# Kernel tuning notes

Hardware: AMD Instinct MI355X
Metric: run time of the kernel (lower is better)

Reference implementation:

```python
import jax, jax.numpy as jnp
import numpy as np

ND, NPR, DD, DP, LAT, AT, B = 2048, 2048, 128, 128, 128, 32, 16384


def setup_inputs():
    key = jax.random.key(0)
    ks = jax.random.split(key, 20)
    s = 0.05
    d = {}
    d["e_p_adj"] = (jax.random.uniform(ks[0], (ND, NPR)) < 0.05).astype(jnp.float32)
    d["e_e_adj"] = (jax.random.uniform(ks[1], (ND, ND)) < 0.05).astype(jnp.float32)
    d["p_p_adj"] = (jax.random.uniform(ks[2], (NPR, NPR)) < 0.05).astype(jnp.float32)
    d["input_disease"] = jax.random.randint(ks[3], (B,), 0, ND)
    d["input_drug"] = jax.random.randint(ks[4], (B,), 0, NPR)
    d["labels"] = jax.random.randint(ks[5], (B,), 0, 2)
    # learned parameters
    d["disease_emb"] = jax.random.normal(ks[6], (ND, DD)) * s
    d["drug_emb"] = jax.random.normal(ks[7], (NPR, DP)) * s
    d["Wdg"] = jax.random.normal(ks[8], (DP, LAT)) * s   # disease_gcn_w
    d["bdg_lin"] = jnp.zeros((LAT,))                      # Linear bias
    d["bdg"] = jnp.zeros((LAT,))                          # extra disease_gcn_b
    d["Wpg"] = jax.random.normal(ks[9], (DD, LAT)) * s   # drug_gcn_w
    d["bpg_lin"] = jnp.zeros((LAT,))
    d["bpg"] = jnp.zeros((LAT,))
    d["Wa1_d"] = jax.random.normal(ks[10], (DP + DD, AT)) * s  # concat [key(drug), query(disease)]
    d["ba1_d"] = jnp.zeros((AT,))
    d["Wa2_d"] = jax.random.normal(ks[11], (AT, 1)) * s
    d["ba2_d"] = jnp.zeros((1,))
    d["Wa1_p"] = jax.random.normal(ks[12], (DD + DP, AT)) * s  # concat [key(disease), query(drug)]
    d["ba1_p"] = jnp.zeros((AT,))
    d["Wa2_p"] = jax.random.normal(ks[13], (AT, 1)) * s
    d["ba2_p"] = jnp.zeros((1,))
    d["Wd2"] = jax.random.normal(ks[14], (DD, LAT)) * s  # disease_w2
    d["bd2"] = jnp.zeros((LAT,))
    d["Wp3"] = jax.random.normal(ks[15], (DP, LAT)) * s  # drug_w3
    d["bp3"] = jnp.zeros((LAT,))
    d["mlp_W1"] = jax.random.normal(ks[16], (LAT, DD)) * s
    d["mlp_b1"] = jnp.zeros((DD,))
    d["mlp_W2"] = jax.random.normal(ks[17], (DD, DD)) * s
    d["mlp_b2"] = jnp.zeros((DD,))
    d["Wpred"] = jax.random.normal(ks[18], (DD, 1)) * s
    d["bpred"] = jnp.zeros((1,))
    return d


def _attention_gcn(adj, other, selfe, W1, b1, W2, b2):
    # torch: concat([key=other, query=self]) -> Linear(W1) ; split W1 instead of
    # materializing the [Ns, No, Dk+Dq] concat tensor (same math, less HBM traffic)
    do = other.shape[1]
    ko = other @ W1[:do]              # [No, A]
    qs = selfe @ W1[do:]              # [Ns, A]
    h = jax.nn.relu(qs[:, None, :] + ko[None, :, :] + b1)   # [Ns, No, A]
    alpha = jax.nn.relu(jnp.squeeze(h @ W2, -1) + b2[0])    # [Ns, No]
    alpha = alpha * adj
    return jax.nn.softmax(alpha, axis=1) @ other            # [Ns, Do]


def _forward(e_p_adj, e_e_adj, p_p_adj, input_disease, input_drug, labels,
             disease_emb, drug_emb, Wdg, bdg_lin, bdg, Wpg, bpg_lin, bpg,
             Wa1_d, ba1_d, Wa2_d, ba2_d, Wa1_p, ba1_p, Wa2_p, ba2_p,
             Wd2, bd2, Wp3, bp3, mlp_W1, mlp_b1, mlp_W2, mlp_b2, Wpred, bpred):
    h_e_gcn = _attention_gcn(e_p_adj, drug_emb, disease_emb, Wa1_d, ba1_d, Wa2_d, ba2_d)
    h_e_gcn = h_e_gcn @ Wdg + bdg_lin + bdg
    h_p_gcn = _attention_gcn(e_p_adj.T, disease_emb, drug_emb, Wa1_p, ba1_p, Wa2_p, ba2_p)
    h_p_gcn = h_p_gcn @ Wpg + bpg_lin + bpg
    # disease knn branch
    deg_d = jnp.sum(e_e_adj, axis=1, keepdims=True) + 1e-8
    h_e_e = ((e_e_adj @ disease_emb) / deg_d) @ Wd2 + bd2
    h_e = jax.nn.selu(h_e_gcn + h_e_e)
    # drug knn branch
    deg_p = jnp.sum(p_p_adj, axis=1, keepdims=True) + 1e-8
    h_p_p = ((p_p_adj @ drug_emb) / deg_p) @ Wp3 + bp3
    h_p = jax.nn.selu(h_p_gcn + h_p_p)
    # pair prediction MLP
    x = h_e[input_disease] * h_p[input_drug]                # [B, LAT]
    x = jax.nn.selu(x @ mlp_W1 + mlp_b1)
    x = jax.nn.selu(x @ mlp_W2 + mlp_b2)
    z = jnp.squeeze(x @ Wpred, -1) + bpred[0]               # [B]
    y = labels.astype(jnp.float32)
    # BCEWithLogitsLoss (stable), mean reduction
    loss = jnp.mean(jnp.maximum(z, 0.0) - z * y + jnp.log1p(jnp.exp(-jnp.abs(z))))
    return (loss, jax.nn.sigmoid(z))


def reference(e_p_adj, e_e_adj, p_p_adj, input_disease, input_drug, labels,
              disease_emb, drug_emb, Wdg, bdg_lin, bdg, Wpg, bpg_lin, bpg,
              Wa1_d, ba1_d, Wa2_d, ba2_d, Wa1_p, ba1_p, Wa2_p, ba2_p,
              Wd2, bd2, Wp3, bp3, mlp_W1, mlp_b1, mlp_W2, mlp_b2, Wpred, bpred):
    return _forward(e_p_adj, e_e_adj, p_p_adj, input_disease, input_drug, labels,
                    disease_emb, drug_emb, Wdg, bdg_lin, bdg, Wpg, bpg_lin, bpg,
                    Wa1_d, ba1_d, Wa2_d, ba2_d, Wa1_p, ba1_p, Wa2_p, ba2_p,
                    Wd2, bd2, Wp3, bp3, mlp_W1, mlp_b1, mlp_W2, mlp_b2, Wpred, bpred)
```

## Files before the change

kernel.cpp:

```cpp
#include <hip/hip_runtime.h>

#define ND   2048
#define BB   16384

typedef unsigned short u16;
typedef unsigned int u32;
typedef __attribute__((ext_vector_type(8))) short short8;
typedef __attribute__((ext_vector_type(4))) float f32x4;

__device__ inline float bf2f(u16 u) {
    union { u32 i; float f; } v; v.i = ((u32)u) << 16; return v.f;
}
__device__ inline u16 f2bf(float f) {
    union { float f; u32 i; } v; v.f = f;
    u32 i = v.i + 0x7fffu + ((v.i >> 16) & 1u);
    return (u16)(i >> 16);
}
__device__ inline float seluf(float x) {
    const float sc = 1.0507009873554805f, al = 1.6732632423543772f;
    return x > 0.f ? sc * x : sc * al * expm1f(x);
}

__global__ void detectk(const void* __restrict__ demb, u32* __restrict__ flag,
                        u32* __restrict__ cntT) {
    const u16* p = (const u16*)demb;
    int tid = threadIdx.x;
    #pragma unroll
    for (int i = 0; i < 8; i++) cntT[i * 256 + tid] = 0u;
    int sane = 0;
    #pragma unroll
    for (int i = 0; i < 2; i++) {
        u16 u = p[4 * tid + 2 * i];
        int e = (u >> 7) & 0xFF;
        if (u == 0 || (e >= 0x66 && e <= 0x8C)) sane++;
    }
    __shared__ int red[256];
    red[tid] = sane; __syncthreads();
    for (int o = 128; o > 0; o >>= 1) {
        if (tid < o) red[tid] += red[tid + o];
        __syncthreads();
    }
    if (tid == 0) flag[0] = (red[0] < 300) ? 1u : 0u;
}

#define NSEG 26
struct CvtArgs { const void* src[NSEG]; int off[NSEG]; int n[NSEG]; };
struct CS {
    const void* adj[3];
    u16* ridx[3]; u32* rcnt[3];
};

__global__ __launch_bounds__(256) void cvtcsr(CvtArgs a, u16* __restrict__ base,
                                              CS c, const u32* __restrict__ flag) {
    int bx = blockIdx.x;
    int t = threadIdx.x;
    bool f32 = flag[0] != 0;
    if (bx < 6144) {
        int m = bx >> 11, r = bx & 2047;
        int lane = t & 63;
        __shared__ u32 lcnt;
        if (t == 0) lcnt = 0;
        __syncthreads();
        float v[8];
        int c0 = t * 8;
        if (f32) {
            const float4* p = (const float4*)((const float*)c.adj[m] + (size_t)r * 2048 + c0);
            float4 x = p[0], y = p[1];
            v[0] = x.x; v[1] = x.y; v[2] = x.z; v[3] = x.w;
            v[4] = y.x; v[5] = y.y; v[6] = y.z; v[7] = y.w;
        } else {
            const uint4* p = (const uint4*)((const u16*)c.adj[m] + (size_t)r * 2048 + c0);
            uint4 x = p[0];
            u32 u[4] = {x.x, x.y, x.z, x.w};
            #pragma unroll
            for (int i = 0; i < 4; i++) {
                v[2 * i + 0] = (u[i] & 0xffffu) ? 1.f : 0.f;
                v[2 * i + 1] = (u[i] >> 16)     ? 1.f : 0.f;
            }
        }
        int cnt = 0;
        #pragma unroll
        for (int i = 0; i < 8; i++) cnt += (v[i] != 0.f) ? 1 : 0;
        int pfx = cnt;
        #pragma unroll
        for (int o = 1; o < 64; o <<= 1) {
            int s = __shfl_up(pfx, o, 64);
            if (lane >= o) pfx += s;
        }
        int wtot = __shfl(pfx, 63, 64);
        u32 wb = 0;
        if (lane == 0) wb = atomicAdd(&lcnt, (u32)wtot);
        wb = __shfl((int)wb, 0, 64);
        int o = (int)wb + pfx - cnt;
        u16* ridx = c.ridx[m] + (size_t)r * 2048;
        #pragma unroll
        for (int i = 0; i < 8; i++) {
            if (v[i] != 0.f) ridx[o++] = (u16)(c0 + i);
        }
        __syncthreads();
        if (t == 0) c.rcnt[m][r] = lcnt;
    } else {
        int idx = bx - 6144;
        int seg = idx >> 6, xb = idx & 63;
        int n = a.n[seg];
        const void* s = a.src[seg];
        u16* d = base + a.off[seg];
        for (int i = xb * 256 + t; i < n; i += 16384)
            d[i] = f32 ? f2bf(((const float*)s)[i]) : ((const u16*)s)[i];
    }
}

struct PR {
    const u16* demb; const u16* pemb;
    const u16* Wa1d; const u16* ba1d;
    const u16* Wa1p; const u16* ba1p;
    float* ko_d; float* qs_d; float* ko_p; float* qs_p;
    const u16* idx0; const u32* cnt0; u16* cidx; u32* ccnt;
    const u16* ts[6]; u16* W1T; u16* W2T; u16* WcTe; u16* WcTp;
    float* cspart;
    const u16* ba[3]; const u16* bb[3]; u16* b_e; u16* b_p;
    float* csd; float* csp;
};

__global__ __launch_bounds__(256) void prep2(PR p) {
    int bx = blockIdx.x;
    int tid = threadIdx.x;
    __shared__ float sx[2][128];
    __shared__ float sred[2][128];
    __shared__ u16 stile[32][33];
    __shared__ float st0[256], st1[256];

    if (bx < 4096) {
        int sub = tid >> 7, t = tid & 127;
        int unit = bx * 2 + sub;
        int row = unit & 2047, m = unit >> 11;
        const u16* src; const u16* W; const u16* bias; float* out;
        switch (m) {
            case 0:  src = p.pemb; W = p.Wa1d;            bias = nullptr; out = p.ko_d; break;
            case 1:  src = p.demb; W = p.Wa1d + 128 * 32; bias = p.ba1d;  out = p.qs_d; break;
            case 2:  src = p.demb; W = p.Wa1p;            bias = nullptr; out = p.ko_p; break;
            default: src = p.pemb; W = p.Wa1p + 128 * 32; bias = p.ba1p;  out = p.qs_p; break;
        }
        sx[sub][t] = bf2f(src[(size_t)row * 128 + t]);
        __syncthreads();
        int a = t & 31, part = t >> 5;
        float s = 0.f;
        #pragma unroll
        for (int k = 0; k < 32; k++)
            s += sx[sub][part * 32 + k] * bf2f(W[(part * 32 + k) * 32 + a]);
        sred[sub][t] = s;
        __syncthreads();
        if (part == 0) {
            float tt = sred[sub][a] + sred[sub][a + 32] + sred[sub][a + 64] + sred[sub][a + 96];
            if (bias) tt += bf2f(bias[a]);
            out[(size_t)row * 32 + a] = tt;
        }
    } else if (bx < 6144) {
        int r = bx - 4096;
        int n = (int)p.cnt0[r];
        const u16* row = p.idx0 + (size_t)r * 2048;
        for (int i = tid; i < n; i += 256) {
            int cc = (int)row[i];
            u32 q = atomicAdd(&p.ccnt[cc], 1u);
            p.cidx[(size_t)cc * 2048 + q] = (u16)r;
        }
    } else if (bx < 6240) {
        int id = bx - 6144;
        int z = id >> 4, rem = id & 15;
        int c0 = (rem & 3) * 32, r0 = (rem >> 2) * 32;
        const u16* in = p.ts[z];
        u16* out; int ldo, ooff;
        switch (z) {
            case 0:  out = p.W1T;  ldo = 128; ooff = 0;   break;
            case 1:  out = p.W2T;  ldo = 128; ooff = 0;   break;
            case 2:  out = p.WcTe; ldo = 256; ooff = 0;   break;
            case 3:  out = p.WcTe; ldo = 256; ooff = 128; break;
            case 4:  out = p.WcTp; ldo = 256; ooff = 0;   break;
            default: out = p.WcTp; ldo = 256; ooff = 128; break;
        }
        int tx = tid & 31, ty = tid >> 5;
        int x = c0 + tx;
        for (int i = ty; i < 32; i += 8)
            stile[i][tx] = in[(size_t)(r0 + i) * 128 + x];
        __syncthreads();
        int rr = r0 + tx;
        for (int i = ty; i < 32; i += 8)
            out[(size_t)(c0 + i) * ldo + ooff + rr] = stile[tx][i];
    } else if (bx < 6304) {
        int id = bx - 6240;
        int m = id >> 5, xb = id & 31;
        const u16* e = m ? p.pemb : p.demb;
        int c2 = tid & 63, rg = tid >> 6;
        int r0 = xb * 64;
        float s0 = 0.f, s1 = 0.f;
        for (int i = 0; i < 16; i++) {
            u32 v = *(const u32*)(e + (size_t)(r0 + i * 4 + rg) * 128 + c2 * 2);
            s0 += bf2f((u16)(v & 0xffffu));
            s1 += bf2f((u16)(v >> 16));
        }
        st0[tid] = s0; st1[tid] = s1;
        __syncthreads();
        if (tid < 64) {
            float a0 = st0[tid] + st0[tid + 64] + st0[tid + 128] + st0[tid + 192];
            float a1 = st1[tid] + st1[tid + 64] + st1[tid + 128] + st1[tid + 192];
            p.cspart[(size_t)m * 4096 + xb * 128 + tid * 2 + 0] = a0;
            p.cspart[(size_t)m * 4096 + xb * 128 + tid * 2 + 1] = a1;
        }
    } else {
    }
}

__global__ void biasfin(PR p) {
    int t = threadIdx.x;
    p.b_e[t] = f2bf(bf2f(p.ba[0][t]) + bf2f(p.ba[1][t]) + bf2f(p.ba[2][t]));
    p.b_p[t] = f2bf(bf2f(p.bb[0][t]) + bf2f(p.bb[1][t]) + bf2f(p.bb[2][t]));
    float sd = 0.f, sp = 0.f;
    for (int b = 0; b < 32; b++) {
        sd += p.cspart[b * 128 + t];
        sp += p.cspart[4096 + b * 128 + t];
    }
    p.csd[t] = sd;
    p.csp[t] = sp;
}

struct SP {
    const u16* idx[4]; const u32* cnt[4];
    const float* ko[4]; const float* qs[4];
    const u16* w2[4]; const u16* b2[4];
    const u16* emb[4]; const float* csum[4];
    u16* out[4]; int ooff[4]; int attn[4];
};

__global__ __launch_bounds__(256) void spagg(SP a) {
    int task = blockIdx.y;
    int tid = threadIdx.x;
    int wv = tid >> 6, lane = tid & 63;
    int grp = lane >> 4, dim = lane & 15;
    int r = blockIdx.x * 4 + wv;
    const u16* idx = a.idx[task] + (size_t)r * 2048;
    int nnz = (int)a.cnt[task][r];
    int isat = a.attn[task];
    const u16* emb = a.emb[task];
    const float* ko = a.ko[task];

    float qsr[32], w2h[32];
    float b2v = 0.f;
    if (isat) {
        const float4* qp = (const float4*)(a.qs[task] + (size_t)r * 32);
        #pragma unroll
        for (int i = 0; i < 8; i++) {
            float4 v = qp[i];
            qsr[4 * i + 0] = v.x; qsr[4 * i + 1] = v.y;
            qsr[4 * i + 2] = v.z; qsr[4 * i + 3] = v.w;
        }
        #pragma unroll
        for (int i = 0; i < 32; i++) w2h[i] = bf2f(a.w2[task][i]);
        b2v = bf2f(a.b2[task][0]);
    }

    float acc[8];
    #pragma unroll
    for (int t = 0; t < 8; t++) acc[t] = 0.f;
    float wsuml = 0.f;

    for (int base = 0; base < nnz; base += 64) {
        int i = base + lane;
        float w = 0.f;
        int j = 0;
        if (i < nnz) {
            j = (int)idx[i];
            if (isat) {
                const float4* kp = (const float4*)(ko + (size_t)j * 32);
                float s = 0.f;
                #pragma unroll
                for (int q = 0; q < 8; q++) {
                    float4 kv = kp[q];
                    s += fmaxf(qsr[4 * q + 0] + kv.x, 0.f) * w2h[4 * q + 0];
                    s += fmaxf(qsr[4 * q + 1] + kv.y, 0.f) * w2h[4 * q + 1];
                    s += fmaxf(qsr[4 * q + 2] + kv.z, 0.f) * w2h[4 * q + 2];
                    s += fmaxf(qsr[4 * q + 3] + kv.w, 0.f) * w2h[4 * q + 3];
                }
                w = __expf(fmaxf(s + b2v, 0.f)) - 1.f;
                wsuml += w;
            }
        }
        int cend = min(64, nnz - base);
        #pragma unroll 4
        for (int k4 = 0; k4 < cend; k4 += 4) {
            int kk = k4 + grp;
            int jk = __shfl(j, kk, 64);
            float wk = isat ? __shfl(w, kk, 64)
                            : ((base + kk < nnz) ? 1.f : 0.f);
            const uint4* pp = (const uint4*)((const char*)emb + jk * 256 + dim * 16);
            uint4 vv = *pp;
            u32 u[4] = {vv.x, vv.y, vv.z, vv.w};
            #pragma unroll
            for (int cc = 0; cc < 4; cc++) {
                acc[2 * cc + 0] = fmaf(wk, bf2f((u16)(u[cc] & 0xffffu)), acc[2 * cc + 0]);
                acc[2 * cc + 1] = fmaf(wk, bf2f((u16)(u[cc] >> 16)), acc[2 * cc + 1]);
            }
        }
    }

    #pragma unroll
    for (int t = 0; t < 8; t++) {
        acc[t] += __shfl_xor(acc[t], 32, 64);
        acc[t] += __shfl_xor(acc[t], 16, 64);
    }
    if (isat) {
        #pragma unroll
        for (int o = 32; o > 0; o >>= 1) wsuml += __shfl_xor(wsuml, o, 64);
    }

    if (grp == 0) {
        float v[8];
        if (isat) {
            float sc = 1.f / (2048.f + wsuml);
            const float* cs = a.csum[task] + dim * 8;
            #pragma unroll
            for (int t = 0; t < 8; t++) v[t] = (cs[t] + acc[t]) * sc;
        } else {
            float sc = 1.f / ((float)nnz + 1e-8f);
            #pragma unroll
            for (int t = 0; t < 8; t++) v[t] = acc[t] * sc;
        }
        uint4 pk;
        pk.x = (u32)f2bf(v[0]) | ((u32)f2bf(v[1]) << 16);
        pk.y = (u32)f2bf(v[2]) | ((u32)f2bf(v[3]) << 16);
        pk.z = (u32)f2bf(v[4]) | ((u32)f2bf(v[5]) << 16);
        pk.w = (u32)f2bf(v[6]) | ((u32)f2bf(v[7]) << 16);
        *(uint4*)(a.out[task] + (size_t)r * 256 + a.ooff[task] + dim * 8) = pk;
    }
}

struct GD4 {
    const void* A[4]; const u16* BT[4]; u16* C[4];
    const u16* bias[4]; const float* rs[4];
    int lda[4], ldb[4], ldc[4], coff[4], kiters[4], act[4], araw[4], rsmode[4];
};

#define PADK 136

__global__ __launch_bounds__(256, 2) void gemmL(GD4 g, const u32* __restrict__ flag) {
    __shared__ __align__(16) u16 As[16][PADK];
    __shared__ __align__(16) u16 Bs[128][PADK];
    int z = blockIdx.y;
    const void* A = g.A[z];
    const u16* BT = g.BT[z];
    int lda = g.lda[z], ldb = g.ldb[z];
    int kiters = g.kiters[z];
    int tid = threadIdx.x;
    int lane = tid & 63, wv = tid >> 6;
    int mrow = lane & 15, quad = lane >> 4;
    int m0 = blockIdx.x * 16;
    int c0 = wv * 32;
    int sr = tid >> 4, sk = (tid & 15) * 8;
    f32x4 acc0 = {0.f, 0.f, 0.f, 0.f}, acc1 = {0.f, 0.f, 0.f, 0.f};

    short8 ra, rb[8];
    auto ldstage = [&](int kb) {
        ra = *(const short8*)((const u16*)A + (size_t)(m0 + sr) * lda + kb + sk);
        const u16* bbase = BT + (size_t)sr * ldb + kb + sk;
        #pragma unroll
        for (int i = 0; i < 8; i++)
            rb[i] = *(const short8*)(bbase + (size_t)i * 16 * ldb);
    };
    auto ststage = [&]() {
        *(short8*)(&As[sr][sk]) = ra;
        #pragma unroll
        for (int i = 0; i < 8; i++)
            *(short8*)(&Bs[i * 16 + sr][sk]) = rb[i];
    };
    auto compute = [&]() {
        #pragma unroll
        for (int ks = 0; ks < 4; ks++) {
            short8 af = *(const short8*)(&As[mrow][ks * 32 + quad * 8]);
            short8 b0 = *(const short8*)(&Bs[c0 + mrow][ks * 32 + quad * 8]);
            short8 b1 = *(const short8*)(&Bs[c0 + 16 + mrow][ks * 32 + quad * 8]);
            acc0 = __builtin_amdgcn_mfma_f32_16x16x32_bf16(af, b0, acc0, 0, 0, 0);
            acc1 = __builtin_amdgcn_mfma_f32_16x16x32_bf16(af, b1, acc1, 0, 0, 0);
        }
    };

    ldstage(0);
    #pragma unroll 1
    for (int it = 0; it < kiters - 1; ++it) {
        ststage();
        __syncthreads();
        ldstage((it + 1) * 128);
        compute();
        __syncthreads();
    }
    ststage();
    __syncthreads();
    compute();

    const float* rs = g.rs[z];
    int rsmode = g.rsmode[z];
    const u16* bi = g.bias[z];
    u16* C = g.C[z];
    int ldc = g.ldc[z], coff = g.coff[z], act = g.act[z];
    int n0 = c0 + mrow, n1 = n0 + 16;
    float bv0 = bi ? bf2f(bi[n0]) : 0.f;
    float bv1 = bi ? bf2f(bi[n1]) : 0.f;
    #pragma unroll
    for (int r = 0; r < 4; r++) {
        int row = m0 + quad * 4 + r;
        float v0 = acc0[r], v1 = acc1[r];
        if (rsmode == 1) { float sc = rs[row]; v0 *= sc; v1 *= sc; }
        else if (rsmode == 2) {
            float t = 0.f;
            #pragma unroll
            for (int p = 0; p < 8; p++) t += rs[row + p * 2048];
            float sc = 1.f / t;
            v0 *= sc; v1 *= sc;
        }
        v0 += bv0; v1 += bv1;
        if (act) { v0 = seluf(v0); v1 = seluf(v1); }
        C[(size_t)row * ldc + coff + n0] = f2bf(v0);
        C[(size_t)row * ldc + coff + n1] = f2bf(v1);
    }
}

#define PADX 136
__global__ __launch_bounds__(256, 2) void mlpfused(
    const u16* __restrict__ he, const u16* __restrict__ hp,
    const int* __restrict__ di, const int* __restrict__ dr,
    const u16* __restrict__ W1T, const u16* __restrict__ b1,
    const u16* __restrict__ W2T, const u16* __restrict__ b2,
    const u16* __restrict__ wpred, const u16* __restrict__ bpred,
    const int* __restrict__ labels,
    float* __restrict__ out, float* __restrict__ part) {
    __shared__ __align__(16) u16 Xs[64][PADX];
    __shared__ __align__(16) u16 Ws[128][PADX];
    __shared__ float wred[4];
    int tid = threadIdx.x;
    int lane = tid & 63, wv = tid >> 6;
    int mrow = lane & 15, quad = lane >> 4;
    int p0 = blockIdx.x * 64;

    {
        int row = tid >> 2, sub = tid & 3;
        int b = p0 + row;
        int ia = di[b], ic = dr[b];
        const uint4* pe = (const uint4*)(he + (size_t)ia * 128 + sub * 32);
        const uint4* pp = (const uint4*)(hp + (size_t)ic * 128 + sub * 32);
        #pragma unroll
        for (int q = 0; q < 4; q++) {
            uint4 ue = pe[q], up = pp[q];
            u32 eu[4] = {ue.x, ue.y, ue.z, ue.w};
            u32 pu[4] = {up.x, up.y, up.z, up.w};
            #pragma unroll
            for (int c = 0; c < 4; c++) {
                float lo = bf2f((u16)(eu[c] & 0xffffu)) * bf2f((u16)(pu[c] & 0xffffu));
                float hi = bf2f((u16)(eu[c] >> 16)) * bf2f((u16)(pu[c] >> 16));
                *(u32*)(&Xs[row][sub * 32 + q * 8 + c * 2]) =
                    (u32)f2bf(lo) | ((u32)f2bf(hi) << 16);
            }
        }
    }
    {
        int n = tid >> 1, half = tid & 1;
        const short8* src = (const short8*)(W1T + (size_t)n * 128 + half * 64);
        short8* dst = (short8*)(&Ws[n][half * 64]);
        #pragma unroll
        for (int i = 0; i < 8; i++) dst[i] = src[i];
    }
    __syncthreads();

    f32x4 acc[8];
    #pragma unroll
    for (int nt = 0; nt < 8; nt++) acc[nt] = {0.f, 0.f, 0.f, 0.f};
    #pragma unroll
    for (int ks = 0; ks < 4; ks++) {
        short8 af = *(const short8*)(&Xs[wv * 16 + mrow][ks * 32 + quad * 8]);
        #pragma unroll
        for (int nt = 0; nt < 8; nt++) {
            short8 bfv = *(const short8*)(&Ws[nt * 16 + mrow][ks * 32 + quad * 8]);
            acc[nt] = __builtin_amdgcn_mfma_f32_16x16x32_bf16(af, bfv, acc[nt], 0, 0, 0);
        }
    }
    __syncthreads();
    #pragma unroll
    for (int nt = 0; nt < 8; nt++) {
        int col = nt * 16 + mrow;
        float bv = bf2f(b1[col]);
        #pragma unroll
        for (int r = 0; r < 4; r++) {
            int row = wv * 16 + quad * 4 + r;
            Xs[row][col] = f2bf(seluf(acc[nt][r] + bv));
        }
    }
    {
        int n = tid >> 1, half = tid & 1;
        const short8* src = (const short8*)(W2T + (size_t)n * 128 + half * 64);
        short8* dst = (short8*)(&Ws[n][half * 64]);
        #pragma unroll
        for (int i = 0; i < 8; i++) dst[i] = src[i];
    }
    __syncthreads();

    #pragma unroll
    for (int nt = 0; nt < 8; nt++) acc[nt] = {0.f, 0.f, 0.f, 0.f};
    #pragma unroll
    for (int ks = 0; ks < 4; ks++) {
        short8 af = *(const short8*)(&Xs[wv * 16 + mrow][ks * 32 + quad * 8]);
        #pragma unroll
        for (int nt = 0; nt < 8; nt++) {
            short8 bfv = *(const short8*)(&Ws[nt * 16 + mrow][ks * 32 + quad * 8]);
            acc[nt] = __builtin_amdgcn_mfma_f32_16x16x32_bf16(af, bfv, acc[nt], 0, 0, 0);
        }
    }

    float zp[4] = {0.f, 0.f, 0.f, 0.f};
    #pragma unroll
    for (int nt = 0; nt < 8; nt++) {
        int col = nt * 16 + mrow;
        float bv = bf2f(b2[col]);
        float wp = bf2f(wpred[col]);
        #pragma unroll
        for (int r = 0; r < 4; r++) {
            float x2 = bf2f(f2bf(seluf(acc[nt][r] + bv)));
            zp[r] = fmaf(x2, wp, zp[r]);
        }
    }
    #pragma unroll
    for (int r = 0; r < 4; r++) {
        #pragma unroll
        for (int o = 1; o < 16; o <<= 1) zp[r] += __shfl_xor(zp[r], o, 64);
    }
    float bpv = bf2f(bpred[0]);
    float lsum = 0.f;
    #pragma unroll
    for (int r = 0; r < 4; r++) {
        int b = p0 + wv * 16 + quad * 4 + r;
        float z = zp[r] + bpv;
        float sig = 1.f / (1.f + __expf(-z));
        if (mrow == 0) out[1 + b] = sig;
        float y = (float)labels[b];
        lsum += fmaxf(z, 0.f) - z * y + log1pf(__expf(-fabsf(z)));
    }
    lsum += __shfl_xor(lsum, 16, 64);
    lsum += __shfl_xor(lsum, 32, 64);
    if (lane == 0) wred[wv] = lsum;
    __syncthreads();
    if (tid == 0) part[blockIdx.x] = wred[0] + wred[1] + wred[2] + wred[3];
}

__global__ void finloss(const float* __restrict__ part, float* __restrict__ out) {
    __shared__ float s[256];
    int t = threadIdx.x;
    s[t] = part[t];
    __syncthreads();
    for (int o = 128; o > 0; o >>= 1) {
        if (t < o) s[t] += s[t + o];
        __syncthreads();
    }
    if (t == 0) out[0] = s[0] * (1.f / 16384.f);
}

extern "C" void kernel_launch(void* const* d_in, const int* in_sizes, int n_in,
                              void* d_out, int out_size, void* d_ws, size_t ws_size,
                              hipStream_t stream) {
    const void* e_p_adj = d_in[0];
    const void* e_e_adj = d_in[1];
    const void* p_p_adj = d_in[2];
    const int* in_dis  = (const int*)d_in[3];
    const int* in_drug = (const int*)d_in[4];
    const int* labels  = (const int*)d_in[5];
    float* out = (float*)d_out;

    char* ws = (char*)d_ws;
    size_t off = 0;
    auto take = [&](size_t bytes) { char* p = ws + off; off = (off + bytes + 255) & ~(size_t)255; return p; };
    u16*   A_e   = (u16*)take((size_t)2048 * 256 * 2);
    u16*   A_p   = (u16*)take((size_t)2048 * 256 * 2);
    u16*   WcTe  = (u16*)take((size_t)128 * 256 * 2);
    u16*   WcTp  = (u16*)take((size_t)128 * 256 * 2);
    u16*   W1T   = (u16*)take((size_t)128 * 128 * 2);
    u16*   W2T   = (u16*)take((size_t)128 * 128 * 2);
    u16*   b_e   = (u16*)take(256);
    u16*   b_p   = (u16*)take(256);
    u16*   h_e   = (u16*)take((size_t)2048 * 128 * 2);
    u16*   h_p   = (u16*)take((size_t)2048 * 128 * 2);
    float* ko_d  = (float*)take((size_t)2048 * 32 * 4);
    float* qs_d  = (float*)take((size_t)2048 * 32 * 4);
    float* ko_p  = (float*)take((size_t)2048 * 32 * 4);
    float* qs_p  = (float*)take((size_t)2048 * 32 * 4);
    float* cspart = (float*)take((size_t)2 * 32 * 128 * 4);
    float* csd   = (float*)take(128 * 4);
    float* csp   = (float*)take(128 * 4);
    float* part  = (float*)take(256 * 4);
    u32*   flag  = (u32*)take(256);
    u16*   canon = (u16*)take((size_t)700000 * 2);
    u16*   idx0  = (u16*)take((size_t)2048 * 2048 * 2);
    u16*   idx1  = (u16*)take((size_t)2048 * 2048 * 2);
    u16*   idx2  = (u16*)take((size_t)2048 * 2048 * 2);
    u16*   idx3  = (u16*)take((size_t)2048 * 2048 * 2);
    u32*   cnt0  = (u32*)take(2048 * 4);
    u32*   cnt2  = (u32*)take(2048 * 4);
    u32*   cnt3  = (u32*)take(2048 * 4);
    u32*   cntT  = (u32*)take(2048 * 4);

    const int segidx[NSEG] = {6, 7, 14, 18, 8, 22, 11, 24, 26, 28,
                              15, 16, 17, 19, 20, 21,
                              9, 10, 12, 13, 23, 25, 27, 29, 30, 31};
    const int segn[NSEG]   = {262144, 262144, 8192, 8192, 16384, 16384, 16384, 16384, 16384, 16384,
                              32, 32, 1, 32, 32, 1,
                              128, 128, 128, 128, 128, 128, 128, 128, 128, 1};
    CvtArgs ca;
    u16* cp[NSEG];
    {
        int o = 0;
        for (int i = 0; i < NSEG; i++) {
            ca.src[i] = d_in[segidx[i]];
            ca.off[i] = o;
            ca.n[i] = segn[i];
            cp[i] = canon + o;
            o += (segn[i] + 15) & ~15;
        }
    }
    u16 *cdemb = cp[0], *cpemb = cp[1], *cWa1d = cp[2], *cWa1p = cp[3];
    u16 *cWdg = cp[4], *cWd2 = cp[5], *cWpg = cp[6], *cWp3 = cp[7];
    u16 *cW1 = cp[8], *cW2 = cp[9];
    u16 *cba1d = cp[10], *cWa2d = cp[11], *cba2d = cp[12];
    u16 *cba1p = cp[13], *cWa2p = cp[14], *cba2p = cp[15];
    u16 *cbdg_lin = cp[16], *cbdg = cp[17], *cbpg_lin = cp[18], *cbpg = cp[19];
    u16 *cbd2 = cp[20], *cbp3 = cp[21], *cmb1 = cp[22], *cmb2 = cp[23];
    u16 *cWpred = cp[24], *cbpred = cp[25];

    detectk<<<1, 256, 0, stream>>>(d_in[6], flag, cntT);

    {
        CS cs;
        cs.adj[0] = e_p_adj; cs.ridx[0] = idx0; cs.rcnt[0] = cnt0;
        cs.adj[1] = e_e_adj; cs.ridx[1] = idx2; cs.rcnt[1] = cnt2;
        cs.adj[2] = p_p_adj; cs.ridx[2] = idx3; cs.rcnt[2] = cnt3;
        cvtcsr<<<6144 + 64 * NSEG, 256, 0, stream>>>(ca, canon, cs, flag);
    }

    PR pr;
    pr.demb = cdemb; pr.pemb = cpemb;
    pr.Wa1d = cWa1d; pr.ba1d = cba1d; pr.Wa1p = cWa1p; pr.ba1p = cba1p;
    pr.ko_d = ko_d; pr.qs_d = qs_d; pr.ko_p = ko_p; pr.qs_p = qs_p;
    pr.idx0 = idx0; pr.cnt0 = cnt0; pr.cidx = idx1; pr.ccnt = cntT;
    pr.ts[0] = cW1; pr.ts[1] = cW2; pr.ts[2] = cWdg;
    pr.ts[3] = cWd2; pr.ts[4] = cWpg; pr.ts[5] = cWp3;
    pr.W1T = W1T; pr.W2T = W2T; pr.WcTe = WcTe; pr.WcTp = WcTp;
    pr.cspart = cspart;
    pr.ba[0] = cbdg_lin; pr.ba[1] = cbdg; pr.ba[2] = cbd2;
    pr.bb[0] = cbpg_lin; pr.bb[1] = cbpg; pr.bb[2] = cbp3;
    pr.b_e = b_e; pr.b_p = b_p; pr.csd = csd; pr.csp = csp;
    prep2<<<6304, 256, 0, stream>>>(pr);
    biasfin<<<1, 128, 0, stream>>>(pr);

    {
        SP sp;
        sp.idx[0] = idx0; sp.cnt[0] = cnt0; sp.ko[0] = ko_d; sp.qs[0] = qs_d;
        sp.w2[0] = cWa2d; sp.b2[0] = cba2d; sp.emb[0] = cpemb; sp.csum[0] = csp;
        sp.out[0] = A_e; sp.ooff[0] = 0; sp.attn[0] = 1;
        sp.idx[1] = idx2; sp.cnt[1] = cnt2; sp.ko[1] = ko_d; sp.qs[1] = qs_d;
        sp.w2[1] = cWa2d; sp.b2[1] = cba2d; sp.emb[1] = cdemb; sp.csum[1] = csd;
        sp.out[1] = A_e; sp.ooff[1] = 128; sp.attn[1] = 0;
        sp.idx[2] = idx1; sp.cnt[2] = cntT; sp.ko[2] = ko_p; sp.qs[2] = qs_p;
        sp.w2[2] = cWa2p; sp.b2[2] = cba2p; sp.emb[2] = cdemb; sp.csum[2] = csd;
        sp.out[2] = A_p; sp.ooff[2] = 0; sp.attn[2] = 1;
        sp.idx[3] = idx3; sp.cnt[3] = cnt3; sp.ko[3] = ko_p; sp.qs[3] = qs_p;
        sp.w2[3] = cWa2p; sp.b2[3] = cba2p; sp.emb[3] = cpemb; sp.csum[3] = csp;
        sp.out[3] = A_p; sp.ooff[3] = 128; sp.attn[3] = 0;
        spagg<<<dim3(512, 4), 256, 0, stream>>>(sp);
    }

    auto setd = [](GD4& g, int z, const void* A, int lda, const u16* BT, int ldb,
                   u16* C, int ldc, int coff, int ki, const u16* bi,
                   const float* rs, int act, int araw, int rm) {
        g.A[z] = A; g.lda[z] = lda; g.BT[z] = BT; g.ldb[z] = ldb;
        g.C[z] = C; g.ldc[z] = ldc; g.coff[z] = coff; g.kiters[z] = ki;
        g.bias[z] = bi; g.rs[z] = rs; g.act[z] = act; g.araw[z] = araw; g.rsmode[z] = rm;
    };

    {
        GD4 g;
        setd(g, 0, A_e, 256, WcTe, 256, h_e, 128, 0, 2, b_e, nullptr, 1, 0, 0);
        setd(g, 1, A_p, 256, WcTp, 256, h_p, 128, 0, 2, b_p, nullptr, 1, 0, 0);
        setd(g, 2, A_e, 256, WcTe, 256, h_e, 128, 0, 2, b_e, nullptr, 1, 0, 0);
        setd(g, 3, A_e, 256, WcTe, 256, h_e, 128, 0, 2, b_e, nullptr, 1, 0, 0);
        gemmL<<<dim3(128, 2), 256, 0, stream>>>(g, flag);
    }

    mlpfused<<<256, 256, 0, stream>>>(h_e, h_p, in_dis, in_drug,
                                      W1T, cmb1, W2T, cmb2,
                                      cWpred, cbpred, labels, out, part);
    finloss<<<1, 256, 0, stream>>>(part, out);
}
```

Before: 236.5 us.

## Fold averaging into prep, batch CSR rows, merge bias/loss finalize kernels

Each CSR-conversion block now handles four adjacency rows instead of one, so the grid shrinks. The non-attention mean aggregations (e_e, p_p) move out of spagg into extra prep2 blocks, leaving spagg with only the two attention tasks. The biasfin kernel is folded into prep2, which now computes column sums in a single pass. The finloss kernel is replaced by an atomic accumulate plus last-block-finishes pattern inside mlpfused. Together these cut kernel launches and idle tails, at the cost of atomic ordering subtleties and a less deterministic loss summation.

```diff
diff --git a/kernel.cpp b/kernel.cpp
--- a/kernel.cpp
+++ b/kernel.cpp
@@ -22,11 +22,13 @@
 }
 
 __global__ void detectk(const void* __restrict__ demb, u32* __restrict__ flag,
-                        u32* __restrict__ cntT) {
+                        u32* __restrict__ cntT, float* __restrict__ lossacc,
+                        u32* __restrict__ losscnt) {
     const u16* p = (const u16*)demb;
     int tid = threadIdx.x;
     #pragma unroll
     for (int i = 0; i < 8; i++) cntT[i * 256 + tid] = 0u;
+    if (tid == 0) { lossacc[0] = 0.f; losscnt[0] = 0u; }
     int sane = 0;
     #pragma unroll
     for (int i = 0; i < 2; i++) {
@@ -55,52 +57,64 @@
     int bx = blockIdx.x;
     int t = threadIdx.x;
     bool f32 = flag[0] != 0;
-    if (bx < 6144) {
-        int m = bx >> 11, r = bx & 2047;
+    if (bx < 1536) {
+        int m = bx >> 9;
+        int r0 = (bx & 511) * 4;
         int lane = t & 63;
-        __shared__ u32 lcnt;
-        if (t == 0) lcnt = 0;
-        __syncthreads();
-        float v[8];
+        __shared__ u32 lcnt[4];
+        if (t < 4) lcnt[t] = 0;
+        __syncthreads();
+        float v[4][8];
         int c0 = t * 8;
         if (f32) {
-            const float4* p = (const float4*)((const float*)c.adj[m] + (size_t)r * 2048 + c0);
-            float4 x = p[0], y = p[1];
-            v[0] = x.x; v[1] = x.y; v[2] = x.z; v[3] = x.w;
-            v[4] = y.x; v[5] = y.y; v[6] = y.z; v[7] = y.w;
+            #pragma unroll
+            for (int rr = 0; rr < 4; rr++) {
+                const float4* p = (const float4*)((const float*)c.adj[m] +
+                                                  (size_t)(r0 + rr) * 2048 + c0);
+                float4 x = p[0], y = p[1];
+                v[rr][0] = x.x; v[rr][1] = x.y; v[rr][2] = x.z; v[rr][3] = x.w;
+                v[rr][4] = y.x; v[rr][5] = y.y; v[rr][6] = y.z; v[rr][7] = y.w;
+            }
         } else {
-            const uint4* p = (const uint4*)((const u16*)c.adj[m] + (size_t)r * 2048 + c0);
-            uint4 x = p[0];
-            u32 u[4] = {x.x, x.y, x.z, x.w};
-            #pragma unroll
-            for (int i = 0; i < 4; i++) {
-                v[2 * i + 0] = (u[i] & 0xffffu) ? 1.f : 0.f;
-                v[2 * i + 1] = (u[i] >> 16)     ? 1.f : 0.f;
+            #pragma unroll
+            for (int rr = 0; rr < 4; rr++) {
+                const uint4* p = (const uint4*)((const u16*)c.adj[m] +
+                                                (size_t)(r0 + rr) * 2048 + c0);
+                uint4 x = p[0];
+                u32 u[4] = {x.x, x.y, x.z, x.w};
+                #pragma unroll
+                for (int i = 0; i < 4; i++) {
+                    v[rr][2 * i + 0] = (u[i] & 0xffffu) ? 1.f : 0.f;
+                    v[rr][2 * i + 1] = (u[i] >> 16)     ? 1.f : 0.f;
+                }
             }
         }
-        int cnt = 0;
-        #pragma unroll
-        for (int i = 0; i < 8; i++) cnt += (v[i] != 0.f) ? 1 : 0;
-        int pfx = cnt;
-        #pragma unroll
-        for (int o = 1; o < 64; o <<= 1) {
-            int s = __shfl_up(pfx, o, 64);
-            if (lane >= o) pfx += s;
-        }
-        int wtot = __shfl(pfx, 63, 64);
-        u32 wb = 0;
-        if (lane == 0) wb = atomicAdd(&lcnt, (u32)wtot);
-        wb = __shfl((int)wb, 0, 64);
-        int o = (int)wb + pfx - cnt;
-        u16* ridx = c.ridx[m] + (size_t)r * 2048;
-        #pragma unroll
-        for (int i = 0; i < 8; i++) {
-            if (v[i] != 0.f) ridx[o++] = (u16)(c0 + i);
-        }
-        __syncthreads();
-        if (t == 0) c.rcnt[m][r] = lcnt;
+        #pragma unroll
+        for (int rr = 0; rr < 4; rr++) {
+            int cnt = 0;
+            #pragma unroll
+            for (int i = 0; i < 8; i++) cnt += (v[rr][i] != 0.f) ? 1 : 0;
+            int pfx = cnt;
+            #pragma unroll
+            for (int o = 1; o < 64; o <<= 1) {
+                int s = __shfl_up(pfx, o, 64);
+                if (lane >= o) pfx += s;
+            }
+            int wtot = __shfl(pfx, 63, 64);
+            u32 wb = 0;
+            if (lane == 0) wb = atomicAdd(&lcnt[rr], (u32)wtot);
+            wb = __shfl((int)wb, 0, 64);
+            int o = (int)wb + pfx - cnt;
+            u16* ridx = c.ridx[m] + (size_t)(r0 + rr) * 2048;
+            #pragma unroll
+            for (int i = 0; i < 8; i++) {
+                if (v[rr][i] != 0.f) ridx[o++] = (u16)(c0 + i);
+            }
+        }
+        __syncthreads();
+        if (t < 4) c.rcnt[m][r0 + t] = lcnt[t];
     } else {
-        int idx = bx - 6144;
+        int idx = bx - 1536;
         int seg = idx >> 6, xb = idx & 63;
         int n = a.n[seg];
         const void* s = a.src[seg];
@@ -117,9 +131,9 @@
     float* ko_d; float* qs_d; float* ko_p; float* qs_p;
     const u16* idx0; const u32* cnt0; u16* cidx; u32* ccnt;
     const u16* ts[6]; u16* W1T; u16* W2T; u16* WcTe; u16* WcTp;
-    float* cspart;
     const u16* ba[3]; const u16* bb[3]; u16* b_e; u16* b_p;
     float* csd; float* csp;
+    const u16* avgidx[2]; const u32* avgcnt[2]; const u16* avgemb[2]; u16* avgout[2];
 };
 
 __global__ __launch_bounds__(256) void prep2(PR p) {
@@ -186,49 +200,93 @@
         int rr = r0 + tx;
         for (int i = ty; i < 32; i += 8)
             out[(size_t)(c0 + i) * ldo + ooff + rr] = stile[tx][i];
-    } else if (bx < 6304) {
+    } else if (bx < 7264) {
         int id = bx - 6240;
-        int m = id >> 5, xb = id & 31;
+        int task = id >> 9, blk = id & 511;
+        int wv = tid >> 6, lane = tid & 63;
+        int grp = lane >> 4, dim = lane & 15;
+        int r = blk * 4 + wv;
+        const u16* idx = p.avgidx[task] + (size_t)r * 2048;
+        int nnz = (int)p.avgcnt[task][r];
+        const u16* emb = p.avgemb[task];
+        float acc[8];
+        #pragma unroll
+        for (int t = 0; t < 8; t++) acc[t] = 0.f;
+        for (int base = 0; base < nnz; base += 64) {
+            int i = base + lane;
+            int j = (i < nnz) ? (int)idx[i] : 0;
+            int cend = min(64, nnz - base);
+            #pragma unroll 4
+            for (int k4 = 0; k4 < cend; k4 += 4) {
+                int kk = k4 + grp;
+                int jk = __shfl(j, kk, 64);
+                float wk = (base + kk < nnz) ? 1.f : 0.f;
+                const uint4* pp = (const uint4*)((const char*)emb + jk * 256 + dim * 16);
+                uint4 vv = *pp;
+                u32 u[4] = {vv.x, vv.y, vv.z, vv.w};
+                #pragma unroll
+                for (int cc = 0; cc < 4; cc++) {
+                    acc[2 * cc + 0] = fmaf(wk, bf2f((u16)(u[cc] & 0xffffu)), acc[2 * cc + 0]);
+                    acc[2 * cc + 1] = fmaf(wk, bf2f((u16)(u[cc] >> 16)), acc[2 * cc + 1]);
+                }
+            }
+        }
+        #pragma unroll
+        for (int t = 0; t < 8; t++) {
+            acc[t] += __shfl_xor(acc[t], 32, 64);
+            acc[t] += __shfl_xor(acc[t], 16, 64);
+        }
+        if (grp == 0) {
+            float sc = 1.f / ((float)nnz + 1e-8f);
+            float v[8];
+            #pragma unroll
+            for (int t = 0; t < 8; t++) v[t] = acc[t] * sc;
+            uint4 pk;
+            pk.x = (u32)f2bf(v[0]) | ((u32)f2bf(v[1]) << 16);
+            pk.y = (u32)f2bf(v[2]) | ((u32)f2bf(v[3]) << 16);
+            pk.z = (u32)f2bf(v[4]) | ((u32)f2bf(v[5]) << 16);
+            pk.w = (u32)f2bf(v[6]) | ((u32)f2bf(v[7]) << 16);
+            *(uint4*)(p.avgout[task] + (size_t)r * 256 + dim * 8) = pk;
+        }
+    } else {
+        int id = bx - 7264;
+        int m = id >> 1, half = id & 1;
         const u16* e = m ? p.pemb : p.demb;
-        int c2 = tid & 63, rg = tid >> 6;
-        int r0 = xb * 64;
+        int c2 = tid & 31, rg = tid >> 5;
+        int dbase = half * 64;
         float s0 = 0.f, s1 = 0.f;
-        for (int i = 0; i < 16; i++) {
-            u32 v = *(const u32*)(e + (size_t)(r0 + i * 4 + rg) * 128 + c2 * 2);
+        for (int it = 0; it < 256; it++) {
+            int row = it * 8 + rg;
+            u32 v = *(const u32*)(e + (size_t)row * 128 + dbase + c2 * 2);
             s0 += bf2f((u16)(v & 0xffffu));
             s1 += bf2f((u16)(v >> 16));
         }
         st0[tid] = s0; st1[tid] = s1;
         __syncthreads();
+        if (tid < 32) {
+            float a0 = 0.f, a1 = 0.f;
+            #pragma unroll
+            for (int g = 0; g < 8; g++) { a0 += st0[g * 32 + tid]; a1 += st1[g * 32 + tid]; }
+            float* cs = m ? p.csp : p.csd;
+            cs[dbase + tid * 2 + 0] = a0;
+            cs[dbase + tid * 2 + 1] = a1;
+        }
         if (tid < 64) {
-            float a0 = st0[tid] + st0[tid + 64] + st0[tid + 128] + st0[tid + 192];
-            float a1 = st1[tid] + st1[tid + 64] + st1[tid + 128] + st1[tid + 192];
-            p.cspart[(size_t)m * 4096 + xb * 128 + tid * 2 + 0] = a0;
-            p.cspart[(size_t)m * 4096 + xb * 128 + tid * 2 + 1] = a1;
-        }
-    } else {
-    }
-}
-
-__global__ void biasfin(PR p) {
-    int t = threadIdx.x;
-    p.b_e[t] = f2bf(bf2f(p.ba[0][t]) + bf2f(p.ba[1][t]) + bf2f(p.ba[2][t]));
-    p.b_p[t] = f2bf(bf2f(p.bb[0][t]) + bf2f(p.bb[1][t]) + bf2f(p.bb[2][t]));
-    float sd = 0.f, sp = 0.f;
-    for (int b = 0; b < 32; b++) {
-        sd += p.cspart[b * 128 + t];
-        sp += p.cspart[4096 + b * 128 + t];
-    }
-    p.csd[t] = sd;
-    p.csp[t] = sp;
+            int d = dbase + tid;
+            if (m == 0)
+                p.b_e[d] = f2bf(bf2f(p.ba[0][d]) + bf2f(p.ba[1][d]) + bf2f(p.ba[2][d]));
+            else
+                p.b_p[d] = f2bf(bf2f(p.bb[0][d]) + bf2f(p.bb[1][d]) + bf2f(p.bb[2][d]));
+        }
+    }
 }
 
 struct SP {
-    const u16* idx[4]; const u32* cnt[4];
-    const float* ko[4]; const float* qs[4];
-    const u16* w2[4]; const u16* b2[4];
-    const u16* emb[4]; const float* csum[4];
-    u16* out[4]; int ooff[4]; int attn[4];
+    const u16* idx[2]; const u32* cnt[2];
+    const float* ko[2]; const float* qs[2];
+    const u16* w2[2]; const u16* b2[2];
+    const u16* emb[2]; const float* csum[2];
+    u16* out[2];
 };
 
 __global__ __launch_bounds__(256) void spagg(SP a) {
@@ -239,13 +297,11 @@
     int r = blockIdx.x * 4 + wv;
     const u16* idx = a.idx[task] + (size_t)r * 2048;
     int nnz = (int)a.cnt[task][r];
-    int isat = a.attn[task];
     const u16* emb = a.emb[task];
     const float* ko = a.ko[task];
 
     float qsr[32], w2h[32];
-    float b2v = 0.f;
-    if (isat) {
+    {
         const float4* qp = (const float4*)(a.qs[task] + (size_t)r * 32);
         #pragma unroll
         for (int i = 0; i < 8; i++) {
@@ -255,8 +311,8 @@
         }
         #pragma unroll
         for (int i = 0; i < 32; i++) w2h[i] = bf2f(a.w2[task][i]);
-        b2v = bf2f(a.b2[task][0]);
-    }
+    }
+    float b2v = bf2f(a.b2[task][0]);
 
     float acc[8];
     #pragma unroll
@@ -269,28 +325,25 @@
         int j = 0;
         if (i < nnz) {
             j = (int)idx[i];
-            if (isat) {
-                const float4* kp = (const float4*)(ko + (size_t)j * 32);
-                float s = 0.f;
-                #pragma unroll
-                for (int q = 0; q < 8; q++) {
-                    float4 kv = kp[q];
-                    s += fmaxf(qsr[4 * q + 0] + kv.x, 0.f) * w2h[4 * q + 0];
-                    s += fmaxf(qsr[4 * q + 1] + kv.y, 0.f) * w2h[4 * q + 1];
-                    s += fmaxf(qsr[4 * q + 2] + kv.z, 0.f) * w2h[4 * q + 2];
-                    s += fmaxf(qsr[4 * q + 3] + kv.w, 0.f) * w2h[4 * q + 3];
-                }
-                w = __expf(fmaxf(s + b2v, 0.f)) - 1.f;
-                wsuml += w;
+            const float4* kp = (const float4*)(ko + (size_t)j * 32);
+            float s = 0.f;
+            #pragma unroll
+            for (int q = 0; q < 8; q++) {
+                float4 kv = kp[q];
+                s += fmaxf(qsr[4 * q + 0] + kv.x, 0.f) * w2h[4 * q + 0];
+                s += fmaxf(qsr[4 * q + 1] + kv.y, 0.f) * w2h[4 * q + 1];
+                s += fmaxf(qsr[4 * q + 2] + kv.z, 0.f) * w2h[4 * q + 2];
+                s += fmaxf(qsr[4 * q + 3] + kv.w, 0.f) * w2h[4 * q + 3];
             }
+            w = __expf(fmaxf(s + b2v, 0.f)) - 1.f;
+            wsuml += w;
         }
         int cend = min(64, nnz - base);
         #pragma unroll 4
         for (int k4 = 0; k4 < cend; k4 += 4) {
             int kk = k4 + grp;
+            float wk = __shfl(w, kk, 64);
             int jk = __shfl(j, kk, 64);
-            float wk = isat ? __shfl(w, kk, 64)
-                            : ((base + kk < nnz) ? 1.f : 0.f);
             const uint4* pp = (const uint4*)((const char*)emb + jk * 256 + dim * 16);
             uint4 vv = *pp;
             u32 u[4] = {vv.x, vv.y, vv.z, vv.w};
@@ -307,29 +360,21 @@
         acc[t] += __shfl_xor(acc[t], 32, 64);
         acc[t] += __shfl_xor(acc[t], 16, 64);
     }
-    if (isat) {
-        #pragma unroll
-        for (int o = 32; o > 0; o >>= 1) wsuml += __shfl_xor(wsuml, o, 64);
-    }
+    #pragma unroll
+    for (int o = 32; o > 0; o >>= 1) wsuml += __shfl_xor(wsuml, o, 64);
 
     if (grp == 0) {
+        float sc = 1.f / (2048.f + wsuml);
+        const float* cs = a.csum[task] + dim * 8;
         float v[8];
-        if (isat) {
-            float sc = 1.f / (2048.f + wsuml);
-            const float* cs = a.csum[task] + dim * 8;
-            #pragma unroll
-            for (int t = 0; t < 8; t++) v[t] = (cs[t] + acc[t]) * sc;
-        } else {
-            float sc = 1.f / ((float)nnz + 1e-8f);
-            #pragma unroll
-            for (int t = 0; t < 8; t++) v[t] = acc[t] * sc;
-        }
+        #pragma unroll
+        for (int t = 0; t < 8; t++) v[t] = (cs[t] + acc[t]) * sc;
         uint4 pk;
         pk.x = (u32)f2bf(v[0]) | ((u32)f2bf(v[1]) << 16);
         pk.y = (u32)f2bf(v[2]) | ((u32)f2bf(v[3]) << 16);
         pk.z = (u32)f2bf(v[4]) | ((u32)f2bf(v[5]) << 16);
         pk.w = (u32)f2bf(v[6]) | ((u32)f2bf(v[7]) << 16);
-        *(uint4*)(a.out[task] + (size_t)r * 256 + a.ooff[task] + dim * 8) = pk;
+        *(uint4*)(a.out[task] + (size_t)r * 256 + dim * 8) = pk;
     }
 }
 
@@ -430,7 +475,8 @@
     const u16* __restrict__ W2T, const u16* __restrict__ b2,
     const u16* __restrict__ wpred, const u16* __restrict__ bpred,
     const int* __restrict__ labels,
-    float* __restrict__ out, float* __restrict__ part) {
+    float* __restrict__ out, float* __restrict__ lossacc,
+    u32* __restrict__ losscnt) {
     __shared__ __align__(16) u16 Xs[64][PADX];
     __shared__ __align__(16) u16 Ws[128][PADX];
     __shared__ float wred[4];
@@ -544,19 +590,16 @@
     lsum += __shfl_xor(lsum, 32, 64);
     if (lane == 0) wred[wv] = lsum;
     __syncthreads();
-    if (tid == 0) part[blockIdx.x] = wred[0] + wred[1] + wred[2] + wred[3];
-}
-
-__global__ void finloss(const float* __restrict__ part, float* __restrict__ out) {
-    __shared__ float s[256];
-    int t = threadIdx.x;
-    s[t] = part[t];
-    __syncthreads();
-    for (int o = 128; o > 0; o >>= 1) {
-        if (t < o) s[t] += s[t + o];
-        __syncthreads();
-    }
-    if (t == 0) out[0] = s[0] * (1.f / 16384.f);
+    if (tid == 0) {
+        float bs = wred[0] + wred[1] + wred[2] + wred[3];
+        atomicAdd(lossacc, bs);
+        __threadfence();
+        u32 old = atomicAdd(losscnt, 1u);
+        if (old == 255u) {
+            float tot = atomicAdd(lossacc, 0.f);
+            out[0] = tot * (1.f / 16384.f);
+        }
+    }
 }
 
 extern "C" void kernel_launch(void* const* d_in, const int* in_sizes, int n_in,
@@ -587,10 +630,10 @@
     float* qs_d  = (float*)take((size_t)2048 * 32 * 4);
     float* ko_p  = (float*)take((size_t)2048 * 32 * 4);
     float* qs_p  = (float*)take((size_t)2048 * 32 * 4);
-    float* cspart = (float*)take((size_t)2 * 32 * 128 * 4);
     float* csd   = (float*)take(128 * 4);
     float* csp   = (float*)take(128 * 4);
-    float* part  = (float*)take(256 * 4);
+    float* lossacc = (float*)take(256);
+    u32*   losscnt = (u32*)((char*)lossacc + 4);
     u32*   flag  = (u32*)take(256);
     u16*   canon = (u16*)take((size_t)700000 * 2);
     u16*   idx0  = (u16*)take((size_t)2048 * 2048 * 2);
@@ -629,14 +672,14 @@
     u16 *cbd2 = cp[20], *cbp3 = cp[21], *cmb1 = cp[22], *cmb2 = cp[23];
     u16 *cWpred = cp[24], *cbpred = cp[25];
 
-    detectk<<<1, 256, 0, stream>>>(d_in[6], flag, cntT);
+    detectk<<<1, 256, 0, stream>>>(d_in[6], flag, cntT, lossacc, losscnt);
 
     {
         CS cs;
         cs.adj[0] = e_p_adj; cs.ridx[0] = idx0; cs.rcnt[0] = cnt0;
         cs.adj[1] = e_e_adj; cs.ridx[1] = idx2; cs.rcnt[1] = cnt2;
         cs.adj[2] = p_p_adj; cs.ridx[2] = idx3; cs.rcnt[2] = cnt3;
-        cvtcsr<<<6144 + 64 * NSEG, 256, 0, stream>>>(ca, canon, cs, flag);
+        cvtcsr<<<1536 + 64 * NSEG, 256, 0, stream>>>(ca, canon, cs, flag);
     }
 
     PR pr;
@@ -647,28 +690,22 @@
     pr.ts[0] = cW1; pr.ts[1] = cW2; pr.ts[2] = cWdg;
     pr.ts[3] = cWd2; pr.ts[4] = cWpg; pr.ts[5] = cWp3;
     pr.W1T = W1T; pr.W2T = W2T; pr.WcTe = WcTe; pr.WcTp = WcTp;
-    pr.cspart = cspart;
     pr.ba[0] = cbdg_lin; pr.ba[1] = cbdg; pr.ba[2] = cbd2;
     pr.bb[0] = cbpg_lin; pr.bb[1] = cbpg; pr.bb[2] = cbp3;
     pr.b_e = b_e; pr.b_p = b_p; pr.csd = csd; pr.csp = csp;
-    prep2<<<6304, 256, 0, stream>>>(pr);
-    biasfin<<<1, 128, 0, stream>>>(pr);
+    pr.avgidx[0] = idx2; pr.avgcnt[0] = cnt2; pr.avgemb[0] = cdemb; pr.avgout[0] = A_e + 128;
+    pr.avgidx[1] = idx3; pr.avgcnt[1] = cnt3; pr.avgemb[1] = cpemb; pr.avgout[1] = A_p + 128;
+    prep2<<<7268, 256, 0, stream>>>(pr);
 
     {
         SP sp;
         sp.idx[0] = idx0; sp.cnt[0] = cnt0; sp.ko[0] = ko_d; sp.qs[0] = qs_d;
         sp.w2[0] = cWa2d; sp.b2[0] = cba2d; sp.emb[0] = cpemb; sp.csum[0] = csp;
-        sp.out[0] = A_e; sp.ooff[0] = 0; sp.attn[0] = 1;
-        sp.idx[1] = idx2; sp.cnt[1] = cnt2; sp.ko[1] = ko_d; sp.qs[1] = qs_d;
-        sp.w2[1] = cWa2d; sp.b2[1] = cba2d; sp.emb[1] = cdemb; sp.csum[1] = csd;
-        sp.out[1] = A_e; sp.ooff[1] = 128; sp.attn[1] = 0;
-        sp.idx[2] = idx1; sp.cnt[2] = cntT; sp.ko[2] = ko_p; sp.qs[2] = qs_p;
-        sp.w2[2] = cWa2p; sp.b2[2] = cba2p; sp.emb[2] = cdemb; sp.csum[2] = csd;
-        sp.out[2] = A_p; sp.ooff[2] = 0; sp.attn[2] = 1;
-        sp.idx[3] = idx3; sp.cnt[3] = cnt3; sp.ko[3] = ko_p; sp.qs[3] = qs_p;
-        sp.w2[3] = cWa2p; sp.b2[3] = cba2p; sp.emb[3] = cpemb; sp.csum[3] = csp;
-        sp.out[3] = A_p; sp.ooff[3] = 128; sp.attn[3] = 0;
-        spagg<<<dim3(512, 4), 256, 0, stream>>>(sp);
+        sp.out[0] = A_e;
+        sp.idx[1] = idx1; sp.cnt[1] = cntT; sp.ko[1] = ko_p; sp.qs[1] = qs_p;
+        sp.w2[1] = cWa2p; sp.b2[1] = cba2p; sp.emb[1] = cdemb; sp.csum[1] = csd;
+        sp.out[1] = A_p;
+        spagg<<<dim3(512, 2), 256, 0, stream>>>(sp);
     }
 
     auto setd = [](GD4& g, int z, const void* A, int lda, const u16* BT, int ldb,
@@ -690,6 +727,6 @@
 
     mlpfused<<<256, 256, 0, stream>>>(h_e, h_p, in_dis, in_drug,
                                       W1T, cmb1, W2T, cmb2,
-                                      cWpred, cbpred, labels, out, part);
-    finloss<<<1, 256, 0, stream>>>(part, out);
-}
+                                      cWpred, cbpred, labels, out,
+                                      lossacc, losscnt);
+}
```

Result: no change. 234.9 us (-0.7%).
